# Performance work log

Hardware: AMD Instinct MI355X
Metric: run time of the kernel (lower is better)

Reference implementation:

```python
import jax, jax.numpy as jnp
import numpy as np

B, N, D = 32768, 50, 128  # batch, neighbours, embedding_dim


def setup_inputs() -> dict:
    key = jax.random.key(0)
    k1, k2, k3, k4 = jax.random.split(key, 4)
    scale = 1.0 / np.sqrt(D)
    return {
        "mainNodeEmbed": jax.random.normal(k1, (B, D), dtype=jnp.float32),
        "neighbourNodesEmbeds": jax.random.normal(k2, (B, N, D), dtype=jnp.float32),
        "W": jax.random.normal(k3, (D, D), dtype=jnp.float32) * scale,            # self.w kernel (no bias)
        "A_w": jax.random.normal(k4, (2 * D, D), dtype=jnp.float32) * scale,      # attentionDense kernel
        "A_b": jnp.zeros((D,), dtype=jnp.float32),                                 # attentionDense bias
    }


def reference(mainNodeEmbed, neighbourNodesEmbeds, W, A_w, A_b):
    # Linear projections (shared weight, no bias)
    px = mainNodeEmbed @ W                       # [B, D]
    pn = neighbourNodesEmbeds @ W                # [B, N, D]
    # mode == 'repeat': tile main node across neighbours, concat on feature dim
    px_rep = jnp.broadcast_to(px[:, None, :], pn.shape)   # [B, N, D]
    cat = jnp.concatenate([px_rep, pn], axis=2)           # [B, N, 2D]
    # attention logits: Dense + leaky_relu (tf default alpha=0.2)
    e_ij = jax.nn.leaky_relu(cat @ A_w + A_b, negative_slope=0.2)  # [B, N, D]
    # softmax over the neighbour axis (axis=1), per feature channel
    a_ij = jax.nn.softmax(e_ij, axis=1)
    # attention-weighted sum over neighbours
    return jnp.sum(a_ij * pn, axis=1)            # [B, D]
```

## Files before the change

kernel.cpp:

```cpp
#include <hip/hip_runtime.h>
#include <math.h>

#define NN 50
#define DD 128
#define MT 4
#define KT 4
#define NIT 64
#define TILE_H 12800

typedef __attribute__((ext_vector_type(4))) float  f32x4;
typedef __attribute__((ext_vector_type(2))) __fp16 f16x2;
typedef __attribute__((ext_vector_type(4))) __fp16 f16x4;
typedef __attribute__((ext_vector_type(8))) __fp16 f16x8;

__device__ float g_WA1f[DD * DD];
__device__ float g_WA2f[DD * DD];
__device__ __attribute__((aligned(16))) __fp16 g_Wt[2 * DD * DD];
__device__ __attribute__((aligned(16))) __fp16 g_W1t[DD * DD];

__global__ void compute_WA(const float* __restrict__ W,
                           const float* __restrict__ A_w) {
    const int d = threadIdx.x, k = blockIdx.x, m = blockIdx.y;
    const float* __restrict__ A = A_w + (size_t)m * DD * DD;
    float acc = 0.f;
#pragma unroll 8
    for (int j = 0; j < DD; ++j)
        acc = fmaf(W[k * DD + j], A[j * DD + d], acc);
    if (m == 0) g_WA1f[k * DD + d] = acc;
    else        g_WA2f[k * DD + d] = acc;
}

__global__ void cvt_weights(const float* __restrict__ W) {
    const int n = blockIdx.x;
    const int k = threadIdx.x;
    if (n < DD)          g_Wt[n * DD + k]             = (__fp16)W[k * DD + n];
    else if (n < 2 * DD) g_Wt[n * DD + k]             = (__fp16)g_WA2f[k * DD + (n - DD)];
    else                 g_W1t[(n - 2 * DD) * DD + k] = (__fp16)g_WA1f[k * DD + (n - 2 * DD)];
}

__device__ __forceinline__ f16x8 cvt8(float4 f0, float4 f1) {
    union { f16x2 h[4]; f16x8 v; } u;
    u.h[0] = __builtin_amdgcn_cvt_pkrtz(f0.x, f0.y);
    u.h[1] = __builtin_amdgcn_cvt_pkrtz(f0.z, f0.w);
    u.h[2] = __builtin_amdgcn_cvt_pkrtz(f1.x, f1.y);
    u.h[3] = __builtin_amdgcn_cvt_pkrtz(f1.z, f1.w);
    return u.v;
}

#define MFMA(a, b, c) __builtin_amdgcn_mfma_f32_16x16x32_f16((a), (b), (c), 0, 0, 0)

__global__ __launch_bounds__(512, 4)
void attn_mfma(const float* __restrict__ x,
               const float* __restrict__ nbr,
               const float* __restrict__ A_b,
               float* __restrict__ out, int B) {
    __shared__ __attribute__((aligned(16))) char tiles[2][TILE_H];
    __shared__ float pxa_lds[NIT][DD];

    const int tid  = threadIdx.x;
    const int w    = tid >> 6;
    const int lane = tid & 63;
    const int c    = lane & 15;
    const int g    = lane >> 4;
    const size_t b0 = (size_t)blockIdx.x * NIT;
    const int col  = 16 * w + c;

    {
        f32x4 pacc[MT];
#pragma unroll
        for (int mt = 0; mt < MT; ++mt) pacc[mt] = (f32x4)0.f;
#pragma unroll
        for (int mt = 0; mt < MT; ++mt) {
            long brow = (long)b0 + 16 * mt + c;
            if (brow > B - 1) brow = B - 1;
            const float4* __restrict__ xp =
                reinterpret_cast<const float4*>(x + brow * DD);
#pragma unroll
            for (int kt = 0; kt < KT; ++kt) {
                const f16x8 a = cvt8(xp[8 * kt + 2 * g], xp[8 * kt + 2 * g + 1]);
                const f16x8 bw = *reinterpret_cast<const f16x8*>(
                    g_W1t + col * DD + 32 * kt + 8 * g);
                pacc[mt] = MFMA(a, bw, pacc[mt]);
            }
        }
        const float ab = A_b[col];
#pragma unroll
        for (int mt = 0; mt < MT; ++mt)
#pragma unroll
            for (int r = 0; r < 4; ++r)
                pxa_lds[16 * mt + 4 * g + r][col] = pacc[mt][r] + ab;
    }

    f16x8 bF[2][KT];
#pragma unroll
    for (int p = 0; p < 2; ++p)
#pragma unroll
        for (int kt = 0; kt < KT; ++kt) {
            bF[p][kt] = *reinterpret_cast<const f16x8*>(
                g_Wt + (p * DD + col) * DD + 32 * kt + 8 * g);
            asm volatile("" : "+v"(bF[p][kt]));
        }

    float4 ra[4];

    auto load_tile = [&](int it) {
        int itc = it < NIT ? it : NIT - 1;
        size_t bidx = b0 + (size_t)itc;
        if (bidx > (size_t)(B - 1)) bidx = (size_t)(B - 1);
        const float4* __restrict__ nb4 =
            reinterpret_cast<const float4*>(nbr + bidx * (size_t)(NN * DD));
#pragma unroll
        for (int j = 0; j < 4; ++j) {
            const int p = w + 8 * j;
            if (p < 25) ra[j] = nb4[p * 64 + lane];
        }
    };

    auto write_tile = [&](char* dst) {
#pragma unroll
        for (int j = 0; j < 4; ++j) {
            const int p = w + 8 * j;
            if (p < 25) {
                const int lb  = p * 512 + lane * 8;
                const int row = lb >> 8;
                const int ad  = lb ^ ((row & 7) << 4);
                union { f16x2 h[2]; f16x4 v; } u;
                u.h[0] = __builtin_amdgcn_cvt_pkrtz(ra[j].x, ra[j].y);
                u.h[1] = __builtin_amdgcn_cvt_pkrtz(ra[j].z, ra[j].w);
                *reinterpret_cast<f16x4*>(dst + ad) = u.v;
            }
        }
    };

    load_tile(0);
    write_tile(tiles[0]);
    load_tile(1);
    asm volatile("s_waitcnt lgkmcnt(0)" ::: "memory");
    __builtin_amdgcn_sched_barrier(0);
    __builtin_amdgcn_s_barrier();

    const float m0v = (g == 0) ? 1.f : 0.f;

#pragma unroll 1
    for (int i = 0; i < NIT; ++i) {
        write_tile(tiles[(i + 1) & 1]);
        load_tile(i + 2);
        __builtin_amdgcn_sched_barrier(0);

        const char* __restrict__ tile = tiles[i & 1];
        f32x4 acc[MT][2];
#pragma unroll
        for (int mt = 0; mt < MT; ++mt)
#pragma unroll
            for (int p = 0; p < 2; ++p) acc[mt][p] = (f32x4)0.f;

#pragma unroll
        for (int mt = 0; mt < MT; ++mt) {
            int row = 16 * mt + c;
            if (row > NN - 1) row = NN - 1;
            const int rb = row * 256;
            const int sw = (row & 7) << 4;
            f16x8 afr[KT];
#pragma unroll
            for (int kt = 0; kt < KT; ++kt)
                afr[kt] = *reinterpret_cast<const f16x8*>(
                    tile + ((rb + kt * 64 + g * 16) ^ sw));
#pragma unroll
            for (int kt = 0; kt < KT; ++kt)
#pragma unroll
                for (int p = 0; p < 2; ++p)
                    acc[mt][p] = MFMA(afr[kt], bF[p][kt], acc[mt][p]);
        }

        {
            const float pxa = pxa_lds[i][col];
            float den = 0.f, num = 0.f;
#pragma unroll
            for (int mt = 0; mt < MT; ++mt)
#pragma unroll
                for (int r = 0; r < 4; ++r) {
                    if (mt == 3 && r >= 2) continue;
                    float t = pxa + acc[mt][1][r];
                    t = fmaxf(t, 0.2f * t);
                    float p = __expf(t);
                    if (mt == 3) p *= m0v;
                    den += p;
                    num = fmaf(p, acc[mt][0][r], num);
                }
            den += __shfl_xor(den, 16); den += __shfl_xor(den, 32);
            num += __shfl_xor(num, 16); num += __shfl_xor(num, 32);
            if (g == 0 && b0 + i < (size_t)B)
                out[(b0 + i) * DD + col] = __fdividef(num, den);
        }

        asm volatile("s_waitcnt lgkmcnt(0)" ::: "memory");
        __builtin_amdgcn_sched_barrier(0);
        __builtin_amdgcn_s_barrier();
    }
}

extern "C" void kernel_launch(void* const* d_in, const int* in_sizes, int n_in,
                              void* d_out, int out_size, void* d_ws, size_t ws_size,
                              hipStream_t stream) {
    const float* x   = (const float*)d_in[0];
    const float* nbr = (const float*)d_in[1];
    const float* W   = (const float*)d_in[2];
    const float* A_w = (const float*)d_in[3];
    const float* A_b = (const float*)d_in[4];
    float* out = (float*)d_out;
    const int B = in_sizes[0] / DD;

    compute_WA<<<dim3(DD, 2), DD, 0, stream>>>(W, A_w);
    cvt_weights<<<3 * DD, DD, 0, stream>>>(W);
    const int grid = (B + NIT - 1) / NIT;
    attn_mfma<<<grid, 512, 0, stream>>>(x, nbr, A_b, out, B);
}
```

Before: 214.9 us.

## Process two tiles per barrier with four-deep LDS buffering and fp16 pxa

Moves to four LDS tile buffers and two register staging sets, so each loop iteration writes two tiles, issues loads for two more, and computes two tiles between barriers. This halves the number of block-wide barriers and keeps more global loads in flight. pxa_lds is stored in fp16 to free LDS for the extra buffers, which costs some precision. The changes raise LDS use to about 67 KB and add registers per thread, which may lower occupancy below the launch-bounds target of 4. The out-of-range guard on the output store is also removed.

```diff
diff --git a/kernel.cpp b/kernel.cpp
--- a/kernel.cpp
+++ b/kernel.cpp
@@ -7,6 +7,7 @@
 #define KT 4
 #define NIT 64
 #define TILE_H 12800
+#define NBUF 4
 
 typedef __attribute__((ext_vector_type(4))) float  f32x4;
 typedef __attribute__((ext_vector_type(2))) __fp16 f16x2;
@@ -54,8 +55,8 @@
                const float* __restrict__ nbr,
                const float* __restrict__ A_b,
                float* __restrict__ out, int B) {
-    __shared__ __attribute__((aligned(16))) char tiles[2][TILE_H];
-    __shared__ float pxa_lds[NIT][DD];
+    __shared__ __attribute__((aligned(16))) char tiles[NBUF][TILE_H];
+    __shared__ __fp16 pxa_lds[NIT][DD];
 
     const int tid  = threadIdx.x;
     const int w    = tid >> 6;
@@ -88,7 +89,7 @@
         for (int mt = 0; mt < MT; ++mt)
 #pragma unroll
             for (int r = 0; r < 4; ++r)
-                pxa_lds[16 * mt + 4 * g + r][col] = pacc[mt][r] + ab;
+                pxa_lds[16 * mt + 4 * g + r][col] = (__fp16)(pacc[mt][r] + ab);
     }
 
     f16x8 bF[2][KT];
@@ -101,9 +102,9 @@
             asm volatile("" : "+v"(bF[p][kt]));
         }
 
-    float4 ra[4];
-
-    auto load_tile = [&](int it) {
+    float4 raA[4], raB[4];
+
+    auto load_tile = [&](float4 (&ra)[4], int it) {
         int itc = it < NIT ? it : NIT - 1;
         size_t bidx = b0 + (size_t)itc;
         if (bidx > (size_t)(B - 1)) bidx = (size_t)(B - 1);
@@ -116,7 +117,7 @@
         }
     };
 
-    auto write_tile = [&](char* dst) {
+    auto write_tile = [&](float4 (&ra)[4], char* dst) {
 #pragma unroll
         for (int j = 0; j < 4; ++j) {
             const int p = w + 8 * j;
@@ -132,22 +133,10 @@
         }
     };
 
-    load_tile(0);
-    write_tile(tiles[0]);
-    load_tile(1);
-    asm volatile("s_waitcnt lgkmcnt(0)" ::: "memory");
-    __builtin_amdgcn_sched_barrier(0);
-    __builtin_amdgcn_s_barrier();
-
     const float m0v = (g == 0) ? 1.f : 0.f;
 
-#pragma unroll 1
-    for (int i = 0; i < NIT; ++i) {
-        write_tile(tiles[(i + 1) & 1]);
-        load_tile(i + 2);
-        __builtin_amdgcn_sched_barrier(0);
-
-        const char* __restrict__ tile = tiles[i & 1];
+    auto compute_tile = [&](int i) {
+        const char* __restrict__ tile = tiles[i & (NBUF - 1)];
         f32x4 acc[MT][2];
 #pragma unroll
         for (int mt = 0; mt < MT; ++mt)
@@ -160,38 +149,55 @@
             if (row > NN - 1) row = NN - 1;
             const int rb = row * 256;
             const int sw = (row & 7) << 4;
-            f16x8 afr[KT];
-#pragma unroll
-            for (int kt = 0; kt < KT; ++kt)
-                afr[kt] = *reinterpret_cast<const f16x8*>(
+#pragma unroll
+            for (int kt = 0; kt < KT; ++kt) {
+                const f16x8 a = *reinterpret_cast<const f16x8*>(
                     tile + ((rb + kt * 64 + g * 16) ^ sw));
-#pragma unroll
-            for (int kt = 0; kt < KT; ++kt)
-#pragma unroll
-                for (int p = 0; p < 2; ++p)
-                    acc[mt][p] = MFMA(afr[kt], bF[p][kt], acc[mt][p]);
-        }
-
-        {
-            const float pxa = pxa_lds[i][col];
-            float den = 0.f, num = 0.f;
-#pragma unroll
-            for (int mt = 0; mt < MT; ++mt)
-#pragma unroll
-                for (int r = 0; r < 4; ++r) {
-                    if (mt == 3 && r >= 2) continue;
-                    float t = pxa + acc[mt][1][r];
-                    t = fmaxf(t, 0.2f * t);
-                    float p = __expf(t);
-                    if (mt == 3) p *= m0v;
-                    den += p;
-                    num = fmaf(p, acc[mt][0][r], num);
-                }
-            den += __shfl_xor(den, 16); den += __shfl_xor(den, 32);
-            num += __shfl_xor(num, 16); num += __shfl_xor(num, 32);
-            if (g == 0 && b0 + i < (size_t)B)
-                out[(b0 + i) * DD + col] = __fdividef(num, den);
-        }
+                acc[mt][0] = MFMA(a, bF[0][kt], acc[mt][0]);
+                acc[mt][1] = MFMA(a, bF[1][kt], acc[mt][1]);
+            }
+        }
+
+        const float pxa = (float)pxa_lds[i][col];
+        float den = 0.f, num = 0.f;
+#pragma unroll
+        for (int mt = 0; mt < MT; ++mt)
+#pragma unroll
+            for (int r = 0; r < 4; ++r) {
+                if (mt == 3 && r >= 2) continue;
+                float t = pxa + acc[mt][1][r];
+                t = fmaxf(t, 0.2f * t);
+                float p = __expf(t);
+                if (mt == 3) p *= m0v;
+                den += p;
+                num = fmaf(p, acc[mt][0][r], num);
+            }
+        den += __shfl_xor(den, 16); den += __shfl_xor(den, 32);
+        num += __shfl_xor(num, 16); num += __shfl_xor(num, 32);
+        if (g == 0)
+            out[(b0 + i) * DD + col] = __fdividef(num, den);
+    };
+
+    load_tile(raA, 0);
+    load_tile(raB, 1);
+    write_tile(raA, tiles[0]);
+    write_tile(raB, tiles[1]);
+    load_tile(raA, 2);
+    load_tile(raB, 3);
+    asm volatile("s_waitcnt lgkmcnt(0)" ::: "memory");
+    __builtin_amdgcn_sched_barrier(0);
+    __builtin_amdgcn_s_barrier();
+
+#pragma unroll 1
+    for (int t0 = 0; t0 < NIT; t0 += 2) {
+        write_tile(raA, tiles[(t0 + 2) & (NBUF - 1)]);
+        write_tile(raB, tiles[(t0 + 3) & (NBUF - 1)]);
+        load_tile(raA, t0 + 4);
+        load_tile(raB, t0 + 5);
+        __builtin_amdgcn_sched_barrier(0);
+
+        compute_tile(t0);
+        compute_tile(t0 + 1);
 
         asm volatile("s_waitcnt lgkmcnt(0)" ::: "memory");
         __builtin_amdgcn_sched_barrier(0);
```

After: 250.1 us. 16.4% more time.
